# Kernel tuning notes

Measured on AMD Instinct MI355X. Metric: run time of the kernel, lower is better.

## Reference

```python
import jax, jax.numpy as jnp
import numpy as np
from jax import lax

Q = 4          # decimation factor
N_ORDER = 8    # IIR filter order (scipy decimate default / explicit n=8)
RP = 0.05      # passband ripple in dB used by scipy.signal.decimate


def _cheby1_ba(N, rp, Wn):
    """Chebyshev type-I lowpass design, identical math to scipy.signal.cheby1."""
    eps = np.sqrt(10.0 ** (0.1 * rp) - 1.0)
    mu = np.arcsinh(1.0 / eps) / N
    k = np.arange(1, N + 1)
    theta = np.pi * (2 * k - 1) / (2 * N)
    # analog prototype poles (cheb1ap)
    p = -np.sinh(mu) * np.sin(theta) + 1j * np.cosh(mu) * np.cos(theta)
    g = np.prod(-p).real
    if N % 2 == 0:
        g /= np.sqrt(1.0 + eps ** 2)
    # frequency pre-warp (iirfilter with fs=2.0)
    fs = 2.0
    warped = 2.0 * fs * np.tan(np.pi * Wn / fs)
    # lp2lp_zpk
    p = p * warped
    g = g * warped ** N
    # bilinear_zpk
    fs2 = 2.0 * fs
    pd = (fs2 + p) / (fs2 - p)
    zd = -np.ones(N)  # N zeros at z=-1
    gd = g * np.real(1.0 / np.prod(fs2 - p))
    b = np.real(gd * np.poly(zd))
    a = np.real(np.poly(pd))
    return b, a


def _lfilter_zi(b, a):
    """Steady-state initial conditions, identical math to scipy.signal.lfilter_zi."""
    n = len(a)
    comp = np.zeros((n - 1, n - 1))
    comp[0, :] = -a[1:] / a[0]
    comp[1:, :-1] = np.eye(n - 2)
    IminusA = np.eye(n - 1) - comp.T
    B = b[1:] - a[1:] * b[0]
    return np.linalg.solve(IminusA, B)


_B_NP, _A_NP = _cheby1_ba(N_ORDER, RP, 0.8 / Q)
_ZI_NP = _lfilter_zi(_B_NP, _A_NP)


def _lfilter(b, a, x, zi):
    """IIR filter, direct-form II transposed. x: (T, M), zi: (order, M)."""
    def step(z, xt):
        yt = b[0] * xt + z[0]                       # (M,)
        z = jnp.concatenate([z[1:], jnp.zeros_like(z[:1])], axis=0) \
            + b[1:, None] * xt[None, :] - a[1:, None] * yt[None, :]
        return z, yt
    _, y = lax.scan(step, zi, x)
    return y


def _filtfilt(b, a, zi, x):
    """scipy.signal.filtfilt with padtype='odd', padlen=3*max(len(a),len(b)). x: (T, M)."""
    edge = 3 * b.shape[0]  # 27 for an order-8 filter
    left = 2.0 * x[0] - x[edge:0:-1]            # odd extension, left
    right = 2.0 * x[-1] - x[-2:-(edge + 2):-1]  # odd extension, right
    ext = jnp.concatenate([left, x, right], axis=0)
    y = _lfilter(b, a, ext, zi[:, None] * ext[0][None, :])          # forward pass
    y = _lfilter(b, a, y[::-1], zi[:, None] * y[-1][None, :])[::-1]  # backward pass
    return y[edge:-edge]


def _decimate(x):
    """scipy.signal.decimate(x, q=Q, n=8, ftype='iir', axis=-1, zero_phase=True)."""
    B_, C_, T = x.shape
    b = jnp.asarray(_B_NP, x.dtype)
    a = jnp.asarray(_A_NP, x.dtype)
    zi = jnp.asarray(_ZI_NP, x.dtype)
    xt = x.reshape(B_ * C_, T).T  # (T, M) -- time leading for lax.scan
    y = _filtfilt(b, a, zi, xt)
    y = y.T.reshape(B_, C_, T)
    return y[..., ::Q]


def setup_inputs() -> dict:
    key = jax.random.key(0)
    x = jax.random.normal(key, (32, 16, 65536), dtype=jnp.float32)
    return {"x": x}


def reference(x):
    return _decimate(x)
```

## Files before the change

### kernel.cpp

```cpp
#include <hip/hip_runtime.h>
#include <cmath>
#include <complex>

namespace {

constexpr int TLEN   = 65536;
constexpr int NCH    = 512;
constexpr size_t YB_ROWS = 16400;
constexpr int PITCH  = 68;


struct Coefs {
  float b0,b1,b2,b3,b4,b5,b6,b7,b8;
  float na1,na2,na3,na4,na5,na6,na7,na8;
  float zi0,zi1,zi2,zi3,zi4,zi5,zi6,zi7;
};

#define IIR_STEP(xv, yv)                                  \
  do {                                                    \
    yv = fmaf(cf.b0, (xv), z0);                           \
    z0 = fmaf(cf.na1, yv, fmaf(cf.b1, (xv), z1));         \
    z1 = fmaf(cf.na2, yv, fmaf(cf.b2, (xv), z2));         \
    z2 = fmaf(cf.na3, yv, fmaf(cf.b3, (xv), z3));         \
    z3 = fmaf(cf.na4, yv, fmaf(cf.b4, (xv), z4));         \
    z4 = fmaf(cf.na5, yv, fmaf(cf.b5, (xv), z5));         \
    z5 = fmaf(cf.na6, yv, fmaf(cf.b6, (xv), z6));         \
    z6 = fmaf(cf.na7, yv, fmaf(cf.b7, (xv), z7));         \
    z7 = fmaf(cf.na8, yv, cf.b8 * (xv));                  \
  } while (0)

template<int QOFF>
__device__ __forceinline__ void run_chunk1(const float* __restrict__ x,
                                           float* __restrict__ yb,
                                           const Coefs& cf,
                                           float (&lds)[2][64 * PITCH],
                                           int m0, int e0, int nsub,
                                           int store_lo, int store_hi) {
  const int lane   = threadIdx.x;
  const int vtbase = e0 - 27;
  const int mIdx   = m0 + lane;
  float4* yq = reinterpret_cast<float4*>(yb);
  const int tq  = lane & 15;
  const int chb = lane >> 4;
  float4 rr[16];

  auto interior = [&](int k) {
    const int vt0 = vtbase + 64 * k;
    return vt0 >= 0 && vt0 + 63 < TLEN;
  };
  auto issue = [&](int k) {
    if (!interior(k)) return;
    const int vt0 = vtbase + 64 * k;
    const float* p = x + (size_t)(m0 + chb) * TLEN + vt0 + 4 * tq;
#pragma unroll
    for (int pp = 0; pp < 16; ++pp)
      rr[pp] = *reinterpret_cast<const float4*>(p + (size_t)(4 * pp) * TLEN);
  };
  auto commit = [&](int k) {
    float* b = lds[k & 1];
    if (interior(k)) {
#pragma unroll
      for (int pp = 0; pp < 16; ++pp)
        *reinterpret_cast<float4*>(&b[(chb + 4 * pp) * PITCH + 4 * tq]) = rr[pp];
    } else {
      const int vt = vtbase + 64 * k + lane;
      const bool lo = vt < 0, hi = vt >= TLEN;
      const int idx  = lo ? -vt : (hi ? 2 * TLEN - 2 - vt : vt);
      const int eidx = hi ? TLEN - 1 : 0;
      const float esc = (lo || hi) ? 2.0f : 0.0f;
      const float msc = (lo || hi) ? -1.0f : 1.0f;
      const float* xr = x + (size_t)m0 * TLEN;
#pragma unroll 8
      for (int ch = 0; ch < 64; ++ch, xr += TLEN)
        b[ch * PITCH + lane] = fmaf(msc, xr[idx], esc * xr[eidx]);
    }
  };

  issue(0); commit(0);

  float z0 = 0, z1 = 0, z2 = 0, z3 = 0, z4 = 0, z5 = 0, z6 = 0, z7 = 0;
  float4 oq = make_float4(0.f, 0.f, 0.f, 0.f);

  for (int k = 0; k < nsub; ++k) {
    if (k + 1 < nsub) issue(k + 1);
    const float* tile = lds[k & 1] + lane * PITCH;
    if (k == 0) {
      float x0 = tile[0];
      z0 = cf.zi0 * x0; z1 = cf.zi1 * x0; z2 = cf.zi2 * x0; z3 = cf.zi3 * x0;
      z4 = cf.zi4 * x0; z5 = cf.zi5 * x0; z6 = cf.zi6 * x0; z7 = cf.zi7 * x0;
    }
#pragma unroll
    for (int j = 0; j < 16; ++j) {
      const float4 xv = *reinterpret_cast<const float4*>(tile + 4 * j);
      const float xs[4] = {xv.x, xv.y, xv.z, xv.w};
#pragma unroll
      for (int d = 0; d < 4; ++d) {
        float yv; IIR_STEP(xs[d], yv);
        if (QOFF == 1) {
          if (k == 0 && j == 0 && d < 3)
            yb[2048 + (size_t)mIdx * 4 + d + 1] = yv;
        }
        const int qq = (4 * j + d + QOFF) & 3;
        if (qq == 0) oq.x = yv;
        else if (qq == 1) oq.y = yv;
        else if (qq == 2) oq.z = yv;
        else {
          oq.w = yv;
          const int step = 64 * k + 4 * j + d;
          if (step >= store_lo && step <= store_hi)
            yq[(size_t)((e0 + step + 5) >> 2) * 512 + mIdx] = oq;
        }
      }
    }
    if (k + 1 < nsub) commit(k + 1);
  }
}

__global__ __launch_bounds__(64) void k_fwd3(const float* __restrict__ x,
                                             float* __restrict__ yb, Coefs cf) {
  __shared__ float lds[2][64 * PITCH];
  const int c  = blockIdx.x;
  const int m0 = blockIdx.y * 64;
  if (c == 0)
    run_chunk1<1>(x, yb, cf, lds, m0, 0, 8, 6, 510);
  else if (c == 127)
    run_chunk1<0>(x, yb, cf, lds, m0, 512 * 127 - 253, 13, 255, 819);
  else
    run_chunk1<0>(x, yb, cf, lds, m0, 512 * c - 253, 12, 255, 763);
}

__global__ __launch_bounds__(256) void k_bwd(const float* __restrict__ yb,
                                             float* __restrict__ ot2, Coefs cf) {
  const int m = blockIdx.y * 256 + threadIdx.x;
  const int c = blockIdx.x;
  const int own_lo = 256 * c;
  float z0, z1, z2, z3, z4, z5, z6, z7;
  int g_begin;
  if (c <= 1) {
    float y0 = yb[(size_t)16398 * 2048 + (size_t)m * 4 + 2];
    z0 = cf.zi0 * y0; z1 = cf.zi1 * y0; z2 = cf.zi2 * y0; z3 = cf.zi3 * y0;
    z4 = cf.zi4 * y0; z5 = cf.zi5 * y0; z6 = cf.zi6 * y0; z7 = cf.zi7 * y0;
#pragma unroll
    for (int s = 65594; s >= 65584; --s) {
      float yin = yb[(size_t)(s >> 2) * 2048 + (size_t)m * 4 + (s & 3)];
      float wv; IIR_STEP(yin, wv);
      (void)wv;
    }
    g_begin = 16395;
  } else {
    g_begin = 16463 - 64 * c;
    float y0 = yb[(size_t)g_begin * 2048 + (size_t)m * 4 + 3];
    z0 = cf.zi0 * y0; z1 = cf.zi1 * y0; z2 = cf.zi2 * y0; z3 = cf.zi3 * y0;
    z4 = cf.zi4 * y0; z5 = cf.zi5 * y0; z6 = cf.zi6 * y0; z7 = cf.zi7 * y0;
  }
  const int g_stop = max(1, 16334 - 64 * c);
  const float4* yv = reinterpret_cast<const float4*>(yb);
  auto ld = [&](int r) {
    int rr = r < 0 ? 0 : r;
    return yv[(size_t)rr * 512 + m];
  };
  float4 b0 = ld(g_begin), b1 = ld(g_begin - 1), b2 = ld(g_begin - 2), b3 = ld(g_begin - 3);
  float4 b4 = ld(g_begin - 4), b5 = ld(g_begin - 5), b6 = ld(g_begin - 6), b7 = ld(g_begin - 7);
  for (int g = g_begin; g >= g_stop; g -= 4) {
    float4 c0 = b0, c1 = b1, c2 = b2, c3 = b3;
    b0 = b4; b1 = b5; b2 = b6; b3 = b7;
    b4 = ld(g - 8); b5 = ld(g - 9); b6 = ld(g - 10); b7 = ld(g - 11);
    float4 pack;
#pragma unroll
    for (int j = 0; j < 4; ++j) {
      float4 q = (j == 0) ? c0 : (j == 1) ? c1 : (j == 2) ? c2 : c3;
      float w3, w2, w1, w0;
      IIR_STEP(q.w, w3);
      IIR_STEP(q.z, w2);
      IIR_STEP(q.y, w1);
      IIR_STEP(q.x, w0);
      (void)w3; (void)w2; (void)w1;
      if (j == 0) pack.w = w0;
      else if (j == 1) pack.z = w0;
      else if (j == 2) pack.y = w0;
      else pack.x = w0;
    }
    if (65594 - 4 * g >= own_lo && g >= 11 && g <= 16391)
      *reinterpret_cast<float4*>(ot2 + (size_t)((g - 11) >> 2) * 2048 + (size_t)m * 4) = pack;
  }
}

__global__ __launch_bounds__(256) void k_outT(const float* __restrict__ ot2,
                                              float* __restrict__ out) {
  __shared__ float4 lds4[64 * 65];
  const int q0 = blockIdx.x * 64;
  const int m0 = blockIdx.y * 64;
  const int tid = threadIdx.x;
#pragma unroll
  for (int i = 0; i < 16; ++i) {
    int idx = tid + i * 256;
    int ql = idx >> 6;
    int ml = idx & 63;
    lds4[ql * 65 + ml] = *reinterpret_cast<const float4*>(
        ot2 + (size_t)(q0 + ql) * 2048 + (size_t)(m0 + ml) * 4);
  }
  __syncthreads();
#pragma unroll
  for (int i = 0; i < 16; ++i) {
    int idx = tid + i * 256;
    int ml = idx >> 6;
    int ql = idx & 63;
    float4 v = lds4[ql * 65 + ml];
    *reinterpret_cast<float4*>(
        out + (size_t)(m0 + ml) * 16384 + (size_t)(q0 + ql) * 4) = v;
  }
}

static void solve8(double Mm[8][9], double* zi) {
  for (int col = 0; col < 8; ++col) {
    int piv = col;
    for (int r = col + 1; r < 8; ++r)
      if (std::fabs(Mm[r][col]) > std::fabs(Mm[piv][col])) piv = r;
    if (piv != col)
      for (int j = 0; j < 9; ++j) { double t = Mm[col][j]; Mm[col][j] = Mm[piv][j]; Mm[piv][j] = t; }
    double d = Mm[col][col];
    for (int j = col; j < 9; ++j) Mm[col][j] /= d;
    for (int r = 0; r < 8; ++r)
      if (r != col) {
        double f = Mm[r][col];
        if (f != 0.0)
          for (int j = col; j < 9; ++j) Mm[r][j] -= f * Mm[col][j];
      }
  }
  for (int i = 0; i < 8; ++i) zi[i] = Mm[i][8];
}

static Coefs make_coefs() {
  using cd = std::complex<double>;
  const int N = 8;
  const double rp = 0.05, Wn = 0.8 / 4.0;
  double eps = std::sqrt(std::pow(10.0, 0.1 * rp) - 1.0);
  double mu = std::asinh(1.0 / eps) / N;
  cd p[8];
  for (int i = 0; i < N; ++i) {
    double th = M_PI * (2.0 * (i + 1) - 1.0) / (2.0 * N);
    p[i] = cd(-std::sinh(mu) * std::sin(th), std::cosh(mu) * std::cos(th));
  }
  cd pr(1.0, 0.0);
  for (int i = 0; i < N; ++i) pr *= -p[i];
  double g = pr.real();
  g /= std::sqrt(1.0 + eps * eps);
  const double fs = 2.0;
  double warped = 2.0 * fs * std::tan(M_PI * Wn / fs);
  for (int i = 0; i < N; ++i) p[i] *= warped;
  g *= std::pow(warped, (double)N);
  const double fs2 = 2.0 * fs;
  cd pd[8], dpr(1.0, 0.0);
  for (int i = 0; i < N; ++i) {
    pd[i] = (cd(fs2, 0.0) + p[i]) / (cd(fs2, 0.0) - p[i]);
    dpr *= (cd(fs2, 0.0) - p[i]);
  }
  double gd = g * (cd(1.0, 0.0) / dpr).real();
  static const double binom[9] = {1, 8, 28, 56, 70, 56, 28, 8, 1};
  double b[9], a[9];
  for (int i = 0; i < 9; ++i) b[i] = gd * binom[i];
  cd cp[9]; cp[0] = cd(1, 0);
  for (int i = 1; i < 9; ++i) cp[i] = cd(0, 0);
  for (int i = 0; i < N; ++i)
    for (int j = i + 1; j >= 1; --j) cp[j] -= pd[i] * cp[j - 1];
  for (int i = 0; i < 9; ++i) a[i] = cp[i].real();
  double Mm[8][9];
  for (int i = 0; i < 8; ++i) {
    for (int j = 0; j < 9; ++j) Mm[i][j] = 0.0;
    Mm[i][0] += a[i + 1];
    Mm[i][i] += 1.0;
    if (i < 7) Mm[i][i + 1] = -1.0;
    Mm[i][8] = b[i + 1] - a[i + 1] * b[0];
  }
  double zi[8];
  solve8(Mm, zi);
  Coefs cf;
  cf.b0 = (float)b[0]; cf.b1 = (float)b[1]; cf.b2 = (float)b[2]; cf.b3 = (float)b[3];
  cf.b4 = (float)b[4]; cf.b5 = (float)b[5]; cf.b6 = (float)b[6]; cf.b7 = (float)b[7];
  cf.b8 = (float)b[8];
  cf.na1 = (float)(-a[1]); cf.na2 = (float)(-a[2]); cf.na3 = (float)(-a[3]);
  cf.na4 = (float)(-a[4]); cf.na5 = (float)(-a[5]); cf.na6 = (float)(-a[6]);
  cf.na7 = (float)(-a[7]); cf.na8 = (float)(-a[8]);
  cf.zi0 = (float)zi[0]; cf.zi1 = (float)zi[1]; cf.zi2 = (float)zi[2]; cf.zi3 = (float)zi[3];
  cf.zi4 = (float)zi[4]; cf.zi5 = (float)zi[5]; cf.zi6 = (float)zi[6]; cf.zi7 = (float)zi[7];
  return cf;
}

}

extern "C" void kernel_launch(void* const* d_in, const int* in_sizes, int n_in,
                              void* d_out, int out_size, void* d_ws, size_t ws_size,
                              hipStream_t stream) {
  (void)in_sizes; (void)n_in; (void)out_size; (void)ws_size;
  const float* x = (const float*)d_in[0];
  float* out = (float*)d_out;
  float* yb  = (float*)d_ws;
  float* ot2 = yb + YB_ROWS * 2048;
  Coefs cf = make_coefs();
  hipLaunchKernelGGL(k_fwd3, dim3(128, NCH / 64), dim3(64), 0, stream, x, yb, cf);
  hipLaunchKernelGGL(k_bwd, dim3(257, 2), dim3(256), 0, stream, yb, ot2, cf);
  hipLaunchKernelGGL(k_outT, dim3(4096 / 64, NCH / 64), dim3(256), 0, stream, ot2, out);
}
```

Before: 353.9 us.

## Slab intermediate buffers per channel tile, XOR-swizzle LDS, XCD-aware block mapping

The intermediate forward and backward buffers are re-laid out so that each 64-channel tile owns a contiguous slab, which keeps accesses local to fewer memory pages and L2 lines. The LDS tile drops its padded pitch in favour of an XOR swizzle to avoid bank conflicts without extra space. Grids become 1-D, with the forward kernel interleaving channel tiles across blocks and the backward kernel remapping block ids so that neighbouring work lands on the same XCD for L2 locality. The remapping arithmetic and the swizzled indexing must stay consistent across all three kernels.

```diff
diff --git a/kernel.cpp b/kernel.cpp
--- a/kernel.cpp
+++ b/kernel.cpp
@@ -7,7 +7,6 @@
 constexpr int TLEN   = 65536;
 constexpr int NCH    = 512;
 constexpr size_t YB_ROWS = 16400;
-constexpr int PITCH  = 68;
 
 
 struct Coefs {
@@ -33,13 +32,14 @@
 __device__ __forceinline__ void run_chunk1(const float* __restrict__ x,
                                            float* __restrict__ yb,
                                            const Coefs& cf,
-                                           float (&lds)[2][64 * PITCH],
-                                           int m0, int e0, int nsub,
+                                           float (&lds)[2][4096],
+                                           int mt, int e0, int nsub,
                                            int store_lo, int store_hi) {
   const int lane   = threadIdx.x;
+  const int m0     = mt * 64;
   const int vtbase = e0 - 27;
-  const int mIdx   = m0 + lane;
   float4* yq = reinterpret_cast<float4*>(yb);
+  const size_t slabq = (size_t)mt * YB_ROWS * 64;
   const int tq  = lane & 15;
   const int chb = lane >> 4;
   float4 rr[16];
@@ -60,8 +60,10 @@
     float* b = lds[k & 1];
     if (interior(k)) {
 #pragma unroll
-      for (int pp = 0; pp < 16; ++pp)
-        *reinterpret_cast<float4*>(&b[(chb + 4 * pp) * PITCH + 4 * tq]) = rr[pp];
+      for (int pp = 0; pp < 16; ++pp) {
+        const int row = chb + 4 * pp;
+        *reinterpret_cast<float4*>(&b[row * 64 + 4 * (tq ^ (row & 15))]) = rr[pp];
+      }
     } else {
       const int vt = vtbase + 64 * k + lane;
       const bool lo = vt < 0, hi = vt >= TLEN;
@@ -72,7 +74,8 @@
       const float* xr = x + (size_t)m0 * TLEN;
 #pragma unroll 8
       for (int ch = 0; ch < 64; ++ch, xr += TLEN)
-        b[ch * PITCH + lane] = fmaf(msc, xr[idx], esc * xr[eidx]);
+        b[ch * 64 + 4 * ((lane >> 2) ^ (ch & 15)) + (lane & 3)] =
+            fmaf(msc, xr[idx], esc * xr[eidx]);
     }
   };
 
@@ -83,22 +86,22 @@
 
   for (int k = 0; k < nsub; ++k) {
     if (k + 1 < nsub) issue(k + 1);
-    const float* tile = lds[k & 1] + lane * PITCH;
+    const float* tile = lds[k & 1] + lane * 64;
     if (k == 0) {
-      float x0 = tile[0];
+      float x0 = tile[4 * (lane & 15)];
       z0 = cf.zi0 * x0; z1 = cf.zi1 * x0; z2 = cf.zi2 * x0; z3 = cf.zi3 * x0;
       z4 = cf.zi4 * x0; z5 = cf.zi5 * x0; z6 = cf.zi6 * x0; z7 = cf.zi7 * x0;
     }
 #pragma unroll
     for (int j = 0; j < 16; ++j) {
-      const float4 xv = *reinterpret_cast<const float4*>(tile + 4 * j);
+      const float4 xv = *reinterpret_cast<const float4*>(tile + 4 * (j ^ (lane & 15)));
       const float xs[4] = {xv.x, xv.y, xv.z, xv.w};
 #pragma unroll
       for (int d = 0; d < 4; ++d) {
         float yv; IIR_STEP(xs[d], yv);
         if (QOFF == 1) {
           if (k == 0 && j == 0 && d < 3)
-            yb[2048 + (size_t)mIdx * 4 + d + 1] = yv;
+            yb[((size_t)mt * YB_ROWS + 1) * 256 + (size_t)lane * 4 + d + 1] = yv;
         }
         const int qq = (4 * j + d + QOFF) & 3;
         if (qq == 0) oq.x = yv;
@@ -108,7 +111,7 @@
           oq.w = yv;
           const int step = 64 * k + 4 * j + d;
           if (step >= store_lo && step <= store_hi)
-            yq[(size_t)((e0 + step + 5) >> 2) * 512 + mIdx] = oq;
+            yq[slabq + (size_t)((e0 + step + 5) >> 2) * 64 + lane] = oq;
         }
       }
     }
@@ -116,40 +119,47 @@
   }
 }
 
-__global__ __launch_bounds__(64) void k_fwd3(const float* __restrict__ x,
+__global__ __launch_bounds__(64) void k_fwd4(const float* __restrict__ x,
                                              float* __restrict__ yb, Coefs cf) {
-  __shared__ float lds[2][64 * PITCH];
-  const int c  = blockIdx.x;
-  const int m0 = blockIdx.y * 64;
+  __shared__ float lds[2][4096];
+  const int mt = blockIdx.x & 7;
+  const int c  = blockIdx.x >> 3;
   if (c == 0)
-    run_chunk1<1>(x, yb, cf, lds, m0, 0, 8, 6, 510);
+    run_chunk1<1>(x, yb, cf, lds, mt, 0, 8, 6, 510);
   else if (c == 127)
-    run_chunk1<0>(x, yb, cf, lds, m0, 512 * 127 - 253, 13, 255, 819);
+    run_chunk1<0>(x, yb, cf, lds, mt, 512 * 127 - 253, 13, 255, 819);
   else
-    run_chunk1<0>(x, yb, cf, lds, m0, 512 * c - 253, 12, 255, 763);
+    run_chunk1<0>(x, yb, cf, lds, mt, 512 * c - 253, 12, 255, 763);
 }
 
 __global__ __launch_bounds__(256) void k_bwd(const float* __restrict__ yb,
                                              float* __restrict__ ot2, Coefs cf) {
-  const int m = blockIdx.y * 256 + threadIdx.x;
-  const int c = blockIdx.x;
+  const int id  = blockIdx.x;
+  const int xcd = id & 7, pos = id >> 3;
+  const int wgid = (xcd < 2 ? xcd * 65 : 130 + (xcd - 2) * 64) + pos;
+  const int c  = wgid % 257;
+  const int by = wgid / 257;
+  const int m  = by * 256 + threadIdx.x;
+  const int mtY = m >> 6, chY = m & 63;
+  const size_t slab  = (size_t)mtY * YB_ROWS * 256;
+  const size_t slabq = (size_t)mtY * YB_ROWS * 64;
   const int own_lo = 256 * c;
   float z0, z1, z2, z3, z4, z5, z6, z7;
   int g_begin;
   if (c <= 1) {
-    float y0 = yb[(size_t)16398 * 2048 + (size_t)m * 4 + 2];
+    float y0 = yb[slab + (size_t)16398 * 256 + (size_t)chY * 4 + 2];
     z0 = cf.zi0 * y0; z1 = cf.zi1 * y0; z2 = cf.zi2 * y0; z3 = cf.zi3 * y0;
     z4 = cf.zi4 * y0; z5 = cf.zi5 * y0; z6 = cf.zi6 * y0; z7 = cf.zi7 * y0;
 #pragma unroll
     for (int s = 65594; s >= 65584; --s) {
-      float yin = yb[(size_t)(s >> 2) * 2048 + (size_t)m * 4 + (s & 3)];
+      float yin = yb[slab + (size_t)(s >> 2) * 256 + (size_t)chY * 4 + (s & 3)];
       float wv; IIR_STEP(yin, wv);
       (void)wv;
     }
     g_begin = 16395;
   } else {
     g_begin = 16463 - 64 * c;
-    float y0 = yb[(size_t)g_begin * 2048 + (size_t)m * 4 + 3];
+    float y0 = yb[slab + (size_t)g_begin * 256 + (size_t)chY * 4 + 3];
     z0 = cf.zi0 * y0; z1 = cf.zi1 * y0; z2 = cf.zi2 * y0; z3 = cf.zi3 * y0;
     z4 = cf.zi4 * y0; z5 = cf.zi5 * y0; z6 = cf.zi6 * y0; z7 = cf.zi7 * y0;
   }
@@ -157,7 +167,7 @@
   const float4* yv = reinterpret_cast<const float4*>(yb);
   auto ld = [&](int r) {
     int rr = r < 0 ? 0 : r;
-    return yv[(size_t)rr * 512 + m];
+    return yv[slabq + (size_t)rr * 64 + chY];
   };
   float4 b0 = ld(g_begin), b1 = ld(g_begin - 1), b2 = ld(g_begin - 2), b3 = ld(g_begin - 3);
   float4 b4 = ld(g_begin - 4), b5 = ld(g_begin - 5), b6 = ld(g_begin - 6), b7 = ld(g_begin - 7);
@@ -181,7 +191,8 @@
       else pack.x = w0;
     }
     if (65594 - 4 * g >= own_lo && g >= 11 && g <= 16391)
-      *reinterpret_cast<float4*>(ot2 + (size_t)((g - 11) >> 2) * 2048 + (size_t)m * 4) = pack;
+      *reinterpret_cast<float4*>(ot2 + ((size_t)mtY * 4096 + (size_t)((g - 11) >> 2)) * 256
+                                 + (size_t)chY * 4) = pack;
   }
 }
 
@@ -189,15 +200,16 @@
                                               float* __restrict__ out) {
   __shared__ float4 lds4[64 * 65];
   const int q0 = blockIdx.x * 64;
-  const int m0 = blockIdx.y * 64;
+  const int my = blockIdx.y;
+  const int m0 = my * 64;
   const int tid = threadIdx.x;
+  const float4* src = reinterpret_cast<const float4*>(ot2) + (size_t)my * 4096 * 64;
 #pragma unroll
   for (int i = 0; i < 16; ++i) {
     int idx = tid + i * 256;
     int ql = idx >> 6;
     int ml = idx & 63;
-    lds4[ql * 65 + ml] = *reinterpret_cast<const float4*>(
-        ot2 + (size_t)(q0 + ql) * 2048 + (size_t)(m0 + ml) * 4);
+    lds4[ql * 65 + ml] = src[(size_t)(q0 + ql) * 64 + ml];
   }
   __syncthreads();
 #pragma unroll
@@ -297,7 +309,7 @@
   float* yb  = (float*)d_ws;
   float* ot2 = yb + YB_ROWS * 2048;
   Coefs cf = make_coefs();
-  hipLaunchKernelGGL(k_fwd3, dim3(128, NCH / 64), dim3(64), 0, stream, x, yb, cf);
-  hipLaunchKernelGGL(k_bwd, dim3(257, 2), dim3(256), 0, stream, yb, ot2, cf);
+  hipLaunchKernelGGL(k_fwd4, dim3(1024), dim3(64), 0, stream, x, yb, cf);
+  hipLaunchKernelGGL(k_bwd, dim3(514), dim3(256), 0, stream, yb, ot2, cf);
   hipLaunchKernelGGL(k_outT, dim3(4096 / 64, NCH / 64), dim3(256), 0, stream, ot2, out);
 }
```

Result: no change. 356.4 us (+0.7%).
